# Optimization experiments

Measured on AMD Instinct MI355X. Metric: run time of the kernel, lower is better.

The kernel has to match this reference:

```python
import jax, jax.numpy as jnp
import numpy as np
from jax import lax

B, CIN, COUT, K, SDIM = 4, 64, 128, 3, 512
D = H = W = 48


def setup_inputs() -> dict:
    key = jax.random.key(0)
    ks = jax.random.split(key, 8)
    inv = lambda n: 1.0 / np.sqrt(n)
    return {
        "x": jax.random.normal(ks[0], (B, CIN, D, H, W), jnp.float32),
        "style": jax.random.normal(ks[1], (B, SDIM), jnp.float32),
        "weight": jax.random.normal(ks[2], (COUT, CIN, K, K, K), jnp.float32),
        "bias": jnp.zeros((COUT,), jnp.float32),
        "w_scale": jax.random.uniform(ks[3], (CIN, SDIM), jnp.float32, -inv(SDIM), inv(SDIM)),
        "b_scale": jnp.zeros((CIN,), jnp.float32),
        "w_shift": jax.random.uniform(ks[4], (CIN, SDIM), jnp.float32, -inv(SDIM), inv(SDIM)),
        "b_shift": jnp.zeros((CIN,), jnp.float32),
        "w_kmod": jax.random.uniform(ks[5], (CIN * K ** 3, SDIM), jnp.float32, -inv(SDIM), inv(SDIM)),
        "b_kmod": jnp.zeros((CIN * K ** 3,), jnp.float32),
    }


def reference(x, style, weight, bias, w_scale, b_scale, w_shift, b_shift, w_kmod, b_kmod):
    # style-based per-channel input modulation: x * (1+scale) + shift
    scale = style @ w_scale.T + b_scale          # [B, CIN]
    shift = style @ w_shift.T + b_shift          # [B, CIN]
    xm = x * (1.0 + scale)[:, :, None, None, None] + shift[:, :, None, None, None]
    # per-sample kernel modulation: weight * (1 + kmod)
    kmod = (style @ w_kmod.T + b_kmod).reshape(B, CIN, K, K, K)
    w = weight[None] * (1.0 + kmod[:, None])     # [B, COUT, CIN, K, K, K]

    def conv_one(xi, wi):
        # xi: [CIN, D, H, W], wi: [COUT, CIN, K, K, K]
        return lax.conv_general_dilated(
            xi[None], wi, window_strides=(1, 1, 1), padding="SAME",
            dimension_numbers=("NCDHW", "OIDHW", "NCDHW"))[0]

    out = jax.vmap(conv_one)(xm, w)              # [B, COUT, D, H, W]
    return out + bias[None, :, None, None, None]
```

## Files before the change

kernel.cpp:

```cpp
#include <hip/hip_runtime.h>
#include <hip/hip_bf16.h>

#define NB   4
#define CIN  64
#define COUT 128
#define SDIM 512
#define DIM  48
#define SP   (DIM*DIM*DIM)
#define TAPS 27
#define KTOT (CIN*TAPS)

#define WS_S1P 0
#define WS_SH  (WS_S1P + NB*CIN)
#define WS_KM  (WS_SH + NB*CIN)
#define XPB_OFF   32768ull
#define XPB_BYTES (4ull*125000ull*64ull*2ull)
#define WSBF_OFF  (XPB_OFF + XPB_BYTES)
#define WSBF_BYTES ((size_t)NB*27*8*128*8*2)

typedef __attribute__((ext_vector_type(4))) float  f32x4;
typedef __attribute__((ext_vector_type(8))) short  short8;
typedef __attribute__((ext_vector_type(8))) unsigned short u16x8;

__device__ __forceinline__ void gld16(const void* g, void* l) {
    __builtin_amdgcn_global_load_lds(
        (const __attribute__((address_space(1))) void*)g,
        (__attribute__((address_space(3))) void*)l, 16, 0, 0);
}

__global__ void modparams_kernel(const float* __restrict__ style,
                                 const float* __restrict__ w_scale, const float* __restrict__ b_scale,
                                 const float* __restrict__ w_shift, const float* __restrict__ b_shift,
                                 const float* __restrict__ w_kmod,  const float* __restrict__ b_kmod,
                                 float* __restrict__ ws) {
    const int ROWS = 2 * CIN + CIN * TAPS;
    int gwave = (blockIdx.x * blockDim.x + threadIdx.x) >> 6;
    int lane  = threadIdx.x & 63;
    if (gwave >= NB * ROWS) return;
    int b = gwave / ROWS;
    int r = gwave % ROWS;

    const float* srow = style + b * SDIM;
    const float* mrow;
    float bias, add = 0.f;
    float* dst;
    if (r < CIN) {
        mrow = w_scale + r * SDIM; bias = b_scale[r];
        dst = ws + WS_S1P + b * CIN + r; add = 1.f;
    } else if (r < 2 * CIN) {
        int c = r - CIN;
        mrow = w_shift + c * SDIM; bias = b_shift[c];
        dst = ws + WS_SH + b * CIN + c;
    } else {
        int t = r - 2 * CIN;
        mrow = w_kmod + t * SDIM; bias = b_kmod[t];
        dst = ws + WS_KM + b * (CIN * TAPS) + t;
    }

    float acc = 0.f;
    for (int k = lane; k < SDIM; k += 64) acc += srow[k] * mrow[k];
    #pragma unroll
    for (int off = 32; off; off >>= 1) acc += __shfl_down(acc, off);
    if (lane == 0) *dst = acc + bias + add;
}

__global__ void build_wsbf2_kernel(const float* __restrict__ weight, const float* __restrict__ ws,
                                   unsigned short* __restrict__ wsbf) {
    int d = blockIdx.x * blockDim.x + threadIdx.x;
    if (d >= NB * 27 * 8 * 128 * 8) return;
    int j   = d & 7;
    int o   = (d >> 3) & 127;
    int s   = (d >> 10) & 7;
    int rem = d >> 13;
    int tau = rem % 27;
    int b   = rem / 27;
    int c   = s * 8 + j;
    float wm = weight[(o * CIN + c) * TAPS + tau] * (1.f + ws[WS_KM + b * KTOT + c * TAPS + tau]);
    __hip_bfloat16 h = __float2bfloat16(wm);
    wsbf[d] = *(unsigned short*)&h;
}

__global__ __launch_bounds__(256) void pad_kernel(const float* __restrict__ x,
                                                  const float* __restrict__ ws,
                                                  unsigned short* __restrict__ xpb) {
    __shared__ unsigned short lxm[48 * 72];
    int bid = blockIdx.x;
    int py = bid % 50;
    int pz = (bid / 50) % 50;
    int b  = bid / 2500;
    int t = threadIdx.x;
    bool interior = (pz >= 1 && pz <= 48 && py >= 1 && py <= 48);
    if (interior) {
        int z = pz - 1, y = py - 1;
        const float* xr = x + (size_t)b * CIN * SP + (size_t)z * (DIM*DIM) + y * DIM;
        for (int i = t; i < 3072; i += 256) {
            int c = i / 48, w = i % 48;
            float v = xr[(size_t)c * SP + w];
            float m = v * ws[WS_S1P + b * CIN + c] + ws[WS_SH + b * CIN + c];
            __hip_bfloat16 h = __float2bfloat16(m);
            lxm[w * 72 + c] = *(unsigned short*)&h;
        }
    }
    __syncthreads();
    unsigned short* dst = xpb + (size_t)b * 8000000ull + ((size_t)pz * 2500 + py * 50) * 64;
    for (int i8 = t; i8 < 400; i8 += 256) {
        int w  = i8 >> 3;
        int c8 = (i8 & 7) * 8;
        u16x8 v = {};
        if (interior && w >= 1 && w <= 48)
            v = *(const u16x8*)&lxm[(w - 1) * 72 + c8];
        *(u16x8*)(dst + i8 * 8) = v;
    }
}

#define HALOPOS 600

#define LOADA(dst, tap_) do {                                                  \
    _Pragma("unroll")                                                          \
    for (int j = 0; j < 8; ++j)                                                \
        dst[j] = *(const short8*)(wA + (size_t)(tap_) * 8192 +                 \
                                  (j >> 2) * 4096 + (j & 3) * 128);            \
} while (0)

#define COMPUTE(A, tap_) do {                                                  \
    int kd_ = (tap_) / 9;                                                      \
    int r9_ = (tap_) - kd_ * 9;                                                \
    int kh_ = r9_ / 3;                                                         \
    int kw_ = r9_ - kh_ * 3;                                                   \
    int pb_ = (wz + kd_) * 100 + (cy + kh_) * 10 + cx + kw_;                   \
    _Pragma("unroll")                                                          \
    for (int ch = 0; ch < 2; ++ch) {                                           \
        short8 bfr[4];                                                         \
        _Pragma("unroll")                                                      \
        for (int nf = 0; nf < 4; ++nf) {                                       \
            int pidx = pb_ + nf * 20;                                          \
            bfr[nf] = *(const short8*)&Bh[pidx * 64 +                          \
                          (((ch * 4 + krow) ^ (pidx & 7)) * 8)];               \
        }                                                                      \
        __builtin_amdgcn_s_setprio(1);                                         \
        _Pragma("unroll")                                                      \
        for (int mf = 0; mf < 4; ++mf) {                                       \
            _Pragma("unroll")                                                  \
            for (int nf = 0; nf < 4; ++nf)                                     \
                acc[mf][nf] = __builtin_amdgcn_mfma_f32_16x16x32_bf16(         \
                    A[ch * 4 + mf], bfr[nf], acc[mf][nf], 0, 0, 0);            \
        }                                                                      \
        __builtin_amdgcn_s_setprio(0);                                         \
    }                                                                          \
} while (0)

__global__ __launch_bounds__(512, 2) void conv_fast4_kernel(
    const unsigned short* __restrict__ xpb,
    const unsigned short* __restrict__ wsbf,
    const float* __restrict__ bias,
    float* __restrict__ out)
{
    __shared__ unsigned short Bh[HALOPOS * 64];

    const int t    = threadIdx.x;
    const int lane = t & 63;
    const int wid  = t >> 6;
    const int wz   = wid & 3;
    const int mh   = wid >> 2;

    int bid0 = blockIdx.x;
    int bid  = (bid0 & 7) * 216 + (bid0 >> 3);
    int tile = bid % 432;
    int b    = bid / 432;
    int tx = tile % 6;
    int ty = (tile / 6) % 6;
    int tz = tile / 36;
    int x0 = tx * 8, y0 = ty * 8, z0 = tz * 4;

    const unsigned short* xb = xpb + (size_t)b * 8000000ull;
    const unsigned short* wb = wsbf + (size_t)b * (27 * 8 * 128 * 8);

    #pragma unroll
    for (int it = 0; it < 10; ++it) {
        int i = it * 512 + t;
        if (i < HALOPOS * 8) {
            int pidx = i >> 3;
            int slot = i & 7;
            int hx = pidx % 10;
            int hy = (pidx / 10) % 10;
            int hz = pidx / 100;
            int srcslot = slot ^ (pidx & 7);
            const unsigned short* g = xb
                + ((size_t)((z0 + hz) * 2500 + (y0 + hy) * 50 + (x0 + hx))) * 64
                + srcslot * 8;
            gld16(g, &Bh[i * 8]);
        }
    }

    const int col  = lane & 15;
    const int krow = lane >> 4;
    const int cy   = col >> 3;
    const int cx   = col & 7;

    const unsigned short* wA = wb + (size_t)(krow * 128 + mh * 64 + col) * 8;

    f32x4 acc[4][4] = {};
    short8 a0[8], a1[8];

    LOADA(a0, 0);
    __syncthreads();

    for (int tp = 0; tp < 26; tp += 2) {
        LOADA(a1, tp + 1);
        COMPUTE(a0, tp);
        LOADA(a0, tp + 2);
        COMPUTE(a1, tp + 1);
    }
    COMPUTE(a0, 26);

    int z = z0 + wz;
    #pragma unroll
    for (int mf = 0; mf < 4; ++mf) {
        f32x4 bv = *(const f32x4*)&bias[mh * 64 + mf * 16 + krow * 4];
        #pragma unroll
        for (int nf = 0; nf < 4; ++nf) {
            int y = y0 + nf * 2 + cy;
            int xx = x0 + cx;
            size_t pbase = (size_t)z * (DIM * DIM) + (size_t)y * DIM + xx;
            f32x4 a = acc[mf][nf];
            #pragma unroll
            for (int r = 0; r < 4; ++r) {
                int o = mh * 64 + mf * 16 + krow * 4 + r;
                out[(size_t)(b * COUT + o) * SP + pbase] = a[r] + bv[r];
            }
        }
    }
}

extern "C" void kernel_launch(void* const* d_in, const int* in_sizes, int n_in,
                              void* d_out, int out_size, void* d_ws, size_t ws_size,
                              hipStream_t stream) {
    const float* x       = (const float*)d_in[0];
    const float* style   = (const float*)d_in[1];
    const float* weight  = (const float*)d_in[2];
    const float* bias    = (const float*)d_in[3];
    const float* w_scale = (const float*)d_in[4];
    const float* b_scale = (const float*)d_in[5];
    const float* w_shift = (const float*)d_in[6];
    const float* b_shift = (const float*)d_in[7];
    const float* w_kmod  = (const float*)d_in[8];
    const float* b_kmod  = (const float*)d_in[9];
    float* out = (float*)d_out;
    float* ws  = (float*)d_ws;

    unsigned short* xpb  = (unsigned short*)((char*)d_ws + XPB_OFF);
    unsigned short* wsbf = (unsigned short*)((char*)d_ws + WSBF_OFF);

    {
        int waves = NB * (2 * CIN + CIN * TAPS);
        int blocks = (waves + 3) / 4;
        modparams_kernel<<<blocks, 256, 0, stream>>>(style, w_scale, b_scale,
                                                     w_shift, b_shift, w_kmod, b_kmod, ws);
    }
    {
        int n = NB * 27 * 8 * 128 * 8;
        build_wsbf2_kernel<<<(n + 255) / 256, 256, 0, stream>>>(weight, ws, wsbf);
    }
    {
        int blocks = NB * 50 * 50;
        pad_kernel<<<blocks, 256, 0, stream>>>(x, ws, xpb);
    }
    {
        int blocks = NB * 432;
        conv_fast4_kernel<<<blocks, 512, 0, stream>>>(xpb, wsbf, bias, out);
    }
}
```

Measured before the change: 237.2 us.

## Switch conv inner loop to 32x32x16 MFMA with pipelined B-fragment loads

Replaces the 16x16x32 bf16 MFMA tiling (4x4 fragments per wave) with 32x32x16 MFMA tiles (2x2 per wave). The weight and halo fragment layouts and the output store mapping are reworked to match. The main loop is fully unrolled and software-pipelined, so LDS B-fragment loads for the next k-slice overlap the current MFMAs. The goal is fewer LDS reads per FLOP and fewer MFMA issues, at the cost of larger accumulator register tiles and a different weight-indexing scheme that must match the build_wsbf layout.

After: 260.8 us. +10.0%, slower.

```diff
diff --git a/kernel.cpp b/kernel.cpp
--- a/kernel.cpp
+++ b/kernel.cpp
@@ -18,9 +18,10 @@
 #define WSBF_OFF  (XPB_OFF + XPB_BYTES)
 #define WSBF_BYTES ((size_t)NB*27*8*128*8*2)
 
-typedef __attribute__((ext_vector_type(4))) float  f32x4;
-typedef __attribute__((ext_vector_type(8))) short  short8;
-typedef __attribute__((ext_vector_type(8))) unsigned short u16x8;
+typedef __attribute__((ext_vector_type(4)))  float f32x4;
+typedef __attribute__((ext_vector_type(16))) float f32x16;
+typedef __attribute__((ext_vector_type(8)))  short short8;
+typedef __attribute__((ext_vector_type(8)))  unsigned short u16x8;
 
 __device__ __forceinline__ void gld16(const void* g, void* l) {
     __builtin_amdgcn_global_load_lds(
@@ -114,42 +115,52 @@
 }
 
 #define HALOPOS 600
-
-#define LOADA(dst, tap_) do {                                                  \
+#define BH_CHUNKS (HALOPOS*8)
+
+#define LOADA32(dst, tap_) do {                                                \
     _Pragma("unroll")                                                          \
-    for (int j = 0; j < 8; ++j)                                                \
-        dst[j] = *(const short8*)(wA + (size_t)(tap_) * 8192 +                 \
-                                  (j >> 2) * 4096 + (j & 3) * 128);            \
-} while (0)
-
-#define COMPUTE(A, tap_) do {                                                  \
-    int kd_ = (tap_) / 9;                                                      \
-    int r9_ = (tap_) - kd_ * 9;                                                \
-    int kh_ = r9_ / 3;                                                         \
-    int kw_ = r9_ - kh_ * 3;                                                   \
-    int pb_ = (wz + kd_) * 100 + (cy + kh_) * 10 + cx + kw_;                   \
+    for (int q = 0; q < 8; ++q)                                                \
+        dst[q] = *(const short8*)(wA + (size_t)(tap_) * 8192 +                 \
+                                  (q >> 1) * 2048 + (q & 1) * 256);            \
+} while (0)
+
+#define LOADB(dst, tap_, ks_) do {                                             \
+    const int kd_ = (tap_) / 9;                                                \
+    const int kh_ = ((tap_) / 3) % 3;                                          \
+    const int kw_ = (tap_) % 3;                                                \
     _Pragma("unroll")                                                          \
-    for (int ch = 0; ch < 2; ++ch) {                                           \
-        short8 bfr[4];                                                         \
+    for (int nt = 0; nt < 2; ++nt) {                                           \
+        int pidx = pbase + kd_ * 100 + kh_ * 10 + kw_ + nt * 40;               \
+        dst[nt] = *(const short8*)&Bh[pidx * 64 +                              \
+                      ((((ks_) * 2 + hi) ^ (pidx & 7)) << 3)];                 \
+    }                                                                          \
+} while (0)
+
+#define MFMA4(A, ks_, bb) do {                                                 \
+    __builtin_amdgcn_s_setprio(1);                                             \
+    _Pragma("unroll")                                                          \
+    for (int mt = 0; mt < 2; ++mt) {                                           \
         _Pragma("unroll")                                                      \
-        for (int nf = 0; nf < 4; ++nf) {                                       \
-            int pidx = pb_ + nf * 20;                                          \
-            bfr[nf] = *(const short8*)&Bh[pidx * 64 +                          \
-                          (((ch * 4 + krow) ^ (pidx & 7)) * 8)];               \
-        }                                                                      \
-        __builtin_amdgcn_s_setprio(1);                                         \
-        _Pragma("unroll")                                                      \
-        for (int mf = 0; mf < 4; ++mf) {                                       \
-            _Pragma("unroll")                                                  \
-            for (int nf = 0; nf < 4; ++nf)                                     \
-                acc[mf][nf] = __builtin_amdgcn_mfma_f32_16x16x32_bf16(         \
-                    A[ch * 4 + mf], bfr[nf], acc[mf][nf], 0, 0, 0);            \
-        }                                                                      \
-        __builtin_amdgcn_s_setprio(0);                                         \
+        for (int nt = 0; nt < 2; ++nt)                                         \
+            acc[mt][nt] = __builtin_amdgcn_mfma_f32_32x32x16_bf16(             \
+                A[(ks_) * 2 + mt], bb[nt], acc[mt][nt], 0, 0, 0);              \
     }                                                                          \
-} while (0)
-
-__global__ __launch_bounds__(512, 2) void conv_fast4_kernel(
+    __builtin_amdgcn_s_setprio(0);                                             \
+} while (0)
+
+#define TAPBODY(Acur, Anxt, t_) do {                                           \
+    if ((t_) < 26) LOADA32(Anxt, (t_) + 1);                                    \
+    LOADB(b1, (t_), 1);                                                        \
+    MFMA4(Acur, 0, b0);                                                        \
+    LOADB(b0, (t_), 2);                                                        \
+    MFMA4(Acur, 1, b1);                                                        \
+    LOADB(b1, (t_), 3);                                                        \
+    MFMA4(Acur, 2, b0);                                                        \
+    if ((t_) < 26) LOADB(b0, (t_) + 1, 0);                                     \
+    MFMA4(Acur, 3, b1);                                                        \
+} while (0)
+
+__global__ __launch_bounds__(512, 2) void conv_fast7_kernel(
     const unsigned short* __restrict__ xpb,
     const unsigned short* __restrict__ wsbf,
     const float* __restrict__ bias,
@@ -178,7 +189,7 @@
     #pragma unroll
     for (int it = 0; it < 10; ++it) {
         int i = it * 512 + t;
-        if (i < HALOPOS * 8) {
+        if (i < BH_CHUNKS) {
             int pidx = i >> 3;
             int slot = i & 7;
             int hx = pidx % 10;
@@ -192,41 +203,43 @@
         }
     }
 
-    const int col  = lane & 15;
-    const int krow = lane >> 4;
-    const int cy   = col >> 3;
-    const int cx   = col & 7;
-
-    const unsigned short* wA = wb + (size_t)(krow * 128 + mh * 64 + col) * 8;
-
-    f32x4 acc[4][4] = {};
-    short8 a0[8], a1[8];
-
-    LOADA(a0, 0);
+    const int hi   = lane >> 5;
+    const int n    = lane & 31;
+    const int cy4  = (n >> 3) & 3;
+    const int cx   = n & 7;
+    const int pbase = wz * 100 + cy4 * 10 + cx;
+
+    const unsigned short* wA = wb + (size_t)(hi * 1024 + (mh * 64 + n) * 8);
+
+    f32x16 acc[2][2] = {};
+    short8 aA[8], aB[8], b0[2], b1[2];
+
+    LOADA32(aA, 0);
     __syncthreads();
 
+    LOADB(b0, 0, 0);
+    #pragma unroll
     for (int tp = 0; tp < 26; tp += 2) {
-        LOADA(a1, tp + 1);
-        COMPUTE(a0, tp);
-        LOADA(a0, tp + 2);
-        COMPUTE(a1, tp + 1);
-    }
-    COMPUTE(a0, 26);
-
-    int z = z0 + wz;
-    #pragma unroll
-    for (int mf = 0; mf < 4; ++mf) {
-        f32x4 bv = *(const f32x4*)&bias[mh * 64 + mf * 16 + krow * 4];
+        TAPBODY(aA, aB, tp);
+        TAPBODY(aB, aA, tp + 1);
+    }
+    TAPBODY(aA, aB, 26);
+
+    int z  = z0 + wz;
+    int xx = x0 + cx;
+    #pragma unroll
+    for (int mt = 0; mt < 2; ++mt) {
         #pragma unroll
-        for (int nf = 0; nf < 4; ++nf) {
-            int y = y0 + nf * 2 + cy;
-            int xx = x0 + cx;
-            size_t pbase = (size_t)z * (DIM * DIM) + (size_t)y * DIM + xx;
-            f32x4 a = acc[mf][nf];
+        for (int q = 0; q < 4; ++q) {
+            int ob = mh * 64 + mt * 32 + q * 8 + hi * 4;
+            f32x4 bv = *(const f32x4*)&bias[ob];
             #pragma unroll
-            for (int r = 0; r < 4; ++r) {
-                int o = mh * 64 + mf * 16 + krow * 4 + r;
-                out[(size_t)(b * COUT + o) * SP + pbase] = a[r] + bv[r];
+            for (int nt = 0; nt < 2; ++nt) {
+                int y = y0 + nt * 4 + cy4;
+                size_t p = (size_t)z * (DIM * DIM) + (size_t)y * DIM + xx;
+                #pragma unroll
+                for (int r = 0; r < 4; ++r)
+                    out[(size_t)(b * COUT + ob + r) * SP + p] = acc[mt][nt][q * 4 + r] + bv[r];
             }
         }
     }
@@ -267,6 +280,6 @@
     }
     {
         int blocks = NB * 432;
-        conv_fast4_kernel<<<blocks, 512, 0, stream>>>(xpb, wsbf, bias, out);
-    }
-}
+        conv_fast7_kernel<<<blocks, 512, 0, stream>>>(xpb, wsbf, bias, out);
+    }
+}
```
